# Optimization experiments

Hardware: AMD Instinct MI355X
Metric: run time of the kernel (lower is better)

The kernel has to match this reference:

```python
import jax, jax.numpy as jnp
import numpy as np

N, B, D_IN, HID = 1024, 8, 256, 256
L, SH, LH, GH = 2, 2, 4, 2
H = SH + LH + GH
DH = HID // H
EPS = 1e-5


def _sinusoidal_pe(n, d):
    pos = np.arange(n, dtype=np.float32)[:, None]
    i = np.arange(d, dtype=np.float32)[None, :]
    angle = pos / np.power(10000.0, (2.0 * np.floor(i / 2.0)) / d)
    pe = np.where((np.arange(d) % 2) == 0, np.sin(angle), np.cos(angle))
    return jnp.asarray(pe, jnp.float32)  # (n, d)


def _ln(x, g, b):
    mu = x.mean(-1, keepdims=True)
    var = ((x - mu) ** 2).mean(-1, keepdims=True)
    return (x - mu) * jax.lax.rsqrt(var + EPS) * g + b


def setup_inputs() -> dict:
    key = jax.random.key(0)
    ks = jax.random.split(key, 16)
    s = 0.02
    inp = {
        "nodes": jax.random.normal(ks[0], (N, B, D_IN), jnp.float32),
        "dist": jax.random.randint(ks[1], (B, N, N), 0, 6, jnp.int32),
        "W_in": jax.random.normal(ks[2], (D_IN, HID), jnp.float32) * s,
        "b_in": jnp.zeros((HID,), jnp.float32),
        "ln_in_g": jnp.ones((HID,), jnp.float32),
        "ln_in_b": jnp.zeros((HID,), jnp.float32),
        "Wqkv": jax.random.normal(ks[3], (L, HID, 3 * HID), jnp.float32) * s,
        "bqkv": jnp.zeros((L, 3 * HID), jnp.float32),
        "Wo": jax.random.normal(ks[4], (L, HID, HID), jnp.float32) * s,
        "bo": jnp.zeros((L, HID), jnp.float32),
        "ln1_g": jnp.ones((L, HID), jnp.float32),
        "ln1_b": jnp.zeros((L, HID), jnp.float32),
        "W1": jax.random.normal(ks[5], (L, HID, 2 * HID), jnp.float32) * s,
        "b1": jnp.zeros((L, 2 * HID), jnp.float32),
        "W2": jax.random.normal(ks[6], (L, 2 * HID, HID), jnp.float32) * s,
        "b2": jnp.zeros((L, HID), jnp.float32),
        "ln2_g": jnp.ones((L, HID), jnp.float32),
        "ln2_b": jnp.zeros((L, HID), jnp.float32),
        "bn_g": jnp.ones((HID,), jnp.float32),
        "bn_b": jnp.zeros((HID,), jnp.float32),
    }
    return inp


def reference(nodes, dist, W_in, b_in, ln_in_g, ln_in_b, Wqkv, bqkv, Wo, bo,
              ln1_g, ln1_b, W1, b1, W2, b2, ln2_g, ln2_b, bn_g, bn_b):
    # positional embedding (sinusoidal, added) + dense + LayerNorm; dropout=eval (identity)
    x = nodes + _sinusoidal_pe(N, D_IN)[:, None, :]          # (N,B,D_IN)
    x = _ln(x @ W_in + b_in, ln_in_g, ln_in_b)               # (N,B,HID)

    # dist_to_mask: per-head-group allowed patterns; True in torch mask = disallowed
    short = (dist == 1)[:, None]                             # (B,1,N,N)
    longm = (dist >= 1)[:, None]
    allowed = jnp.concatenate([
        jnp.broadcast_to(short, (B, SH, N, N)),
        jnp.broadcast_to(longm, (B, LH, N, N)),
        jnp.ones((B, GH, N, N), bool),
    ], axis=1)                                               # (B,H,N,N)
    bias = jnp.where(allowed, 0.0, -jnp.inf).astype(x.dtype)

    scale = 1.0 / np.sqrt(DH)
    for l in range(L):
        qkv = x @ Wqkv[l] + bqkv[l]                          # (N,B,3*HID)
        q, k, v = jnp.split(qkv, 3, axis=-1)
        def heads(t):  # (N,B,HID) -> (B,H,N,DH)
            return t.reshape(N, B, H, DH).transpose(1, 2, 0, 3)
        q, k, v = heads(q), heads(k), heads(v)
        s = jnp.einsum('bhnd,bhmd->bhnm', q, k) * scale + bias
        a = jax.nn.softmax(s, axis=-1)
        o = jnp.einsum('bhnm,bhmd->bhnd', a, v)              # (B,H,N,DH)
        o = o.transpose(2, 0, 1, 3).reshape(N, B, HID)
        x = _ln(x + o @ Wo[l] + bo[l], ln1_g[l], ln1_b[l])   # post-norm
        f = jax.nn.relu(x @ W1[l] + b1[l]) @ W2[l] + b2[l]
        x = _ln(x + f, ln2_g[l], ln2_b[l])

    y = x[0]                                                 # (B,HID) first position
    mu = y.mean(0)
    var = ((y - mu) ** 2).mean(0)
    return (y - mu) * jax.lax.rsqrt(var + EPS) * bn_g + bn_b
```

## Files before the change

### kernel.cpp

```cpp
#include <hip/hip_runtime.h>
#include <math.h>

constexpr int Nn = 1024, Bb = 8, HIDc = 256, Hh = 8, DHc = 32;

typedef __bf16 bf16x8 __attribute__((ext_vector_type(8)));
typedef __bf16 bf16x4 __attribute__((ext_vector_type(4)));
typedef float  f32x4  __attribute__((ext_vector_type(4)));

struct WCvtArgs {
    const float* src[9];
    int K[9], M[9], dstOff[9], tiles[9];
};

__global__ __launch_bounds__(256)
void prep_k(WCvtArgs a, __bf16* __restrict__ Wt,
            const int* __restrict__ dist, unsigned char* __restrict__ mp,
            const float* __restrict__ nodes, __bf16* __restrict__ xinb)
{
    __shared__ float ts[32][33];
    const int tid = threadIdx.x;
    if (blockIdx.x < 1088) {
        int bid = blockIdx.x, i = 0;
        while (bid >= a.tiles[i]) { bid -= a.tiles[i]; ++i; }
        const int K = a.K[i], M = a.M[i];
        const int tilesM = M >> 5;
        const int m0 = (bid % tilesM) << 5, k0 = (bid / tilesM) << 5;
        const float* src = a.src[i];
        __bf16* dst = Wt + a.dstOff[i];
        const int tx = tid & 31, ty = tid >> 5;
        #pragma unroll
        for (int j = 0; j < 4; ++j)
            ts[ty + 8 * j][tx] = src[(size_t)(k0 + ty + 8 * j) * M + m0 + tx];
        __syncthreads();
        #pragma unroll
        for (int j = 0; j < 4; ++j)
            dst[(size_t)(m0 + ty + 8 * j) * K + k0 + tx] = (__bf16)ts[tx][ty + 8 * j];
    } else if (blockIdx.x < 3136) {
        const int idx = (blockIdx.x - 1088) * 256 + tid;
        const int quad = idx & 3, c = (idx >> 2) & 15, q = (idx >> 6) & 1023, b = idx >> 16;
        const int* dp = dist + ((((size_t)b << 10) + q) << 10) + c * 64 + quad * 4;
        uchar4 out;
        unsigned char* po = &out.x;
        #pragma unroll
        for (int t = 0; t < 4; ++t) {
            const int4 v = *(const int4*)(dp + t * 16);
            unsigned int code = 0;
            const int dd[4] = {v.x, v.y, v.z, v.w};
            #pragma unroll
            for (int r = 0; r < 4; ++r)
                code |= ((dd[r] == 1 ? 1u : 0u) | (dd[r] >= 1 ? 2u : 0u)) << (2 * r);
            po[t] = (unsigned char)code;
        }
        *(uchar4*)(mp + ((((size_t)b << 10) + q) << 8) + (c << 4) + (quad << 2)) = out;
    } else {
        const int idx = (blockIdx.x - 3136) * 256 + tid;
        const int token = idx >> 7, k2 = (idx & 127) * 2;
        const int b = token >> 10, n = token & 1023;
        const float e = (float)k2 * (1.0f / 256.0f);
        const float freq = exp2f(-13.287712379549449f * e);
        const float ang = (float)n * freq;
        const float2 nd = *(const float2*)(nodes + ((size_t)(n * 8 + b)) * 256 + k2);
        __bf16* p = xinb + (size_t)token * 256 + k2;
        p[0] = (__bf16)(nd.x + sinf(ang));
        p[1] = (__bf16)(nd.y + cosf(ang));
    }
}

template<int NCH>
__device__ __forceinline__ void gemm4(const bf16x8* af, const __bf16* __restrict__ wsrc,
                                      __bf16 (*wlds)[256][72], int mrow, int kcol,
                                      int cq, int col, int quad, f32x4* acc)
{
    constexpr int K = NCH * 64;
    bf16x8 wreg[8];
    #pragma unroll
    for (int i = 0; i < 8; ++i)
        wreg[i] = *(const bf16x8*)(wsrc + (size_t)(i * 32 + mrow) * K + kcol);
    __syncthreads();
    #pragma unroll
    for (int i = 0; i < 8; ++i)
        *(bf16x8*)&wlds[0][i * 32 + mrow][kcol] = wreg[i];
    if (NCH > 1) {
        #pragma unroll
        for (int i = 0; i < 8; ++i)
            wreg[i] = *(const bf16x8*)(wsrc + (size_t)(i * 32 + mrow) * K + 64 + kcol);
    }
    __syncthreads();
    #pragma unroll
    for (int t = 0; t < 4; ++t) acc[t] = (f32x4){0.f, 0.f, 0.f, 0.f};
    for (int ck = 0; ck < NCH; ++ck) {
        #pragma unroll
        for (int t = 0; t < 4; ++t)
            #pragma unroll
            for (int kc = 0; kc < 2; ++kc) {
                const bf16x8 bfr = *(const bf16x8*)(&wlds[ck & 1][cq * 64 + t * 16 + col][kc * 32 + quad * 8]);
                acc[t] = __builtin_amdgcn_mfma_f32_16x16x32_bf16(af[ck * 2 + kc], bfr, acc[t], 0, 0, 0);
            }
        if (ck + 1 < NCH) {
            #pragma unroll
            for (int i = 0; i < 8; ++i)
                *(bf16x8*)&wlds[(ck + 1) & 1][i * 32 + mrow][kcol] = wreg[i];
            if (ck + 2 < NCH) {
                #pragma unroll
                for (int i = 0; i < 8; ++i)
                    wreg[i] = *(const bf16x8*)(wsrc + (size_t)(i * 32 + mrow) * K + (ck + 2) * 64 + kcol);
            }
        }
        __syncthreads();
    }
}

template<bool RESID, bool FFN, bool QKV, bool N0ROWS, bool XGATE, bool BNOUT>
__global__ __launch_bounds__(256)
void layer_k(const __bf16* __restrict__ Ain, const float* __restrict__ xres,
             const __bf16* __restrict__ w0, const float* __restrict__ b0,
             const float* __restrict__ g1, const float* __restrict__ be1,
             const __bf16* __restrict__ w1, const float* __restrict__ b1_,
             const __bf16* __restrict__ w2, const float* __restrict__ b2_,
             const float* __restrict__ g2, const float* __restrict__ be2,
             const __bf16* __restrict__ wq, const float* __restrict__ bq, int qfull,
             const float* __restrict__ bng, const float* __restrict__ bnb,
             float* __restrict__ xout,
             __bf16* __restrict__ qb, __bf16* __restrict__ kb, __bf16* __restrict__ vtb)
{
    __shared__ char smem[73728];
    __bf16 (*wlds)[256][72] = (__bf16 (*)[256][72])smem;
    __bf16 (*trans)[520] = (__bf16 (*)[520])smem;
    __shared__ float red[4][16][2];

    const int tid = threadIdx.x;
    const int lane = tid & 63;
    const int cq = tid >> 6;
    const int col = lane & 15, quad = lane >> 4;
    const int row0 = blockIdx.x * 16;
    const int rowL = col;
    const int mrow = tid >> 3, kcol = (tid & 7) * 8;

    const int rowAg = N0ROWS ? ((col & 7) << 10) : (row0 + col);

    bf16x8 afA[8];
    #pragma unroll
    for (int kc = 0; kc < 8; ++kc)
        afA[kc] = *(const bf16x8*)(Ain + (size_t)rowAg * 256 + kc * 32 + quad * 8);
    f32x4 acc[4];
    gemm4<4>(afA, w0, wlds, mrow, kcol, cq, col, quad, acc);

    float val[4][4];
    {
        float bb[4], gm[4], bt[4];
        #pragma unroll
        for (int t = 0; t < 4; ++t) {
            const int cc = cq * 64 + t * 16 + col;
            bb[t] = b0[cc]; gm[t] = g1[cc]; bt[t] = be1[cc];
        }
        #pragma unroll
        for (int r = 0; r < 4; ++r) {
            const int rl = quad * 4 + r;
            const int rg = N0ROWS ? ((rl & 7) << 10) : (row0 + rl);
            float s1 = 0.f, s2 = 0.f;
            #pragma unroll
            for (int t = 0; t < 4; ++t) {
                float v = acc[t][r] + bb[t];
                if (RESID) v += xres[(size_t)rg * 256 + cq * 64 + t * 16 + col];
                val[r][t] = v; s1 += v; s2 += v * v;
            }
            s1 += __shfl_xor(s1, 1); s1 += __shfl_xor(s1, 2);
            s1 += __shfl_xor(s1, 4); s1 += __shfl_xor(s1, 8);
            s2 += __shfl_xor(s2, 1); s2 += __shfl_xor(s2, 2);
            s2 += __shfl_xor(s2, 4); s2 += __shfl_xor(s2, 8);
            if (col == 0) { red[cq][rl][0] = s1; red[cq][rl][1] = s2; }
        }
        __syncthreads();
        #pragma unroll
        for (int r = 0; r < 4; ++r) {
            const int rl = quad * 4 + r;
            const float s1 = red[0][rl][0] + red[1][rl][0] + red[2][rl][0] + red[3][rl][0];
            const float s2 = red[0][rl][1] + red[1][rl][1] + red[2][rl][1] + red[3][rl][1];
            const float mu = s1 * (1.0f / 256.0f);
            const float rv = rsqrtf(s2 * (1.0f / 256.0f) - mu * mu + 1e-5f);
            #pragma unroll
            for (int t = 0; t < 4; ++t) {
                const float o = (val[r][t] - mu) * rv * gm[t] + bt[t];
                val[r][t] = o;
                trans[rl][cq * 64 + t * 16 + col] = (__bf16)o;
                if (!FFN)
                    xout[(size_t)(row0 + rl) * 256 + cq * 64 + t * 16 + col] = o;
            }
        }
        __syncthreads();
    }

    if (FFN) {
        bf16x8 af1[8];
        #pragma unroll
        for (int kc = 0; kc < 8; ++kc)
            af1[kc] = *(const bf16x8*)(&trans[rowL][kc * 32 + quad * 8]);
        bf16x4 h1p[2][4];
        #pragma unroll
        for (int mh = 0; mh < 2; ++mh) {
            f32x4 accb[4];
            gemm4<4>(af1, w1 + (size_t)mh * 256 * 256, wlds, mrow, kcol, cq, col, quad, accb);
            #pragma unroll
            for (int t = 0; t < 4; ++t) {
                const float bbv = b1_[mh * 256 + cq * 64 + t * 16 + col];
                #pragma unroll
                for (int r = 0; r < 4; ++r)
                    h1p[mh][t][r] = (__bf16)fmaxf(accb[t][r] + bbv, 0.f);
            }
        }
        __syncthreads();
        #pragma unroll
        for (int mh = 0; mh < 2; ++mh)
            #pragma unroll
            for (int t = 0; t < 4; ++t)
                #pragma unroll
                for (int r = 0; r < 4; ++r)
                    trans[quad * 4 + r][mh * 256 + cq * 64 + t * 16 + col] = h1p[mh][t][r];
        __syncthreads();

        bf16x8 af2[16];
        #pragma unroll
        for (int kc = 0; kc < 16; ++kc)
            af2[kc] = *(const bf16x8*)(&trans[rowL][kc * 32 + quad * 8]);
        f32x4 accc[4];
        gemm4<8>(af2, w2, wlds, mrow, kcol, cq, col, quad, accc);

        float bb[4], gm[4], bt[4];
        #pragma unroll
        for (int t = 0; t < 4; ++t) {
            const int cc = cq * 64 + t * 16 + col;
            bb[t] = b2_[cc]; gm[t] = g2[cc]; bt[t] = be2[cc];
        }
        #pragma unroll
        for (int r = 0; r < 4; ++r) {
            const int rl = quad * 4 + r;
            float s1 = 0.f, s2 = 0.f;
            #pragma unroll
            for (int t = 0; t < 4; ++t) {
                const float v = accc[t][r] + bb[t] + val[r][t];
                val[r][t] = v; s1 += v; s2 += v * v;
            }
            s1 += __shfl_xor(s1, 1); s1 += __shfl_xor(s1, 2);
            s1 += __shfl_xor(s1, 4); s1 += __shfl_xor(s1, 8);
            s2 += __shfl_xor(s2, 1); s2 += __shfl_xor(s2, 2);
            s2 += __shfl_xor(s2, 4); s2 += __shfl_xor(s2, 8);
            if (col == 0) { red[cq][rl][0] = s1; red[cq][rl][1] = s2; }
        }
        __syncthreads();
        #pragma unroll
        for (int r = 0; r < 4; ++r) {
            const int rl = quad * 4 + r;
            const float s1 = red[0][rl][0] + red[1][rl][0] + red[2][rl][0] + red[3][rl][0];
            const float s2 = red[0][rl][1] + red[1][rl][1] + red[2][rl][1] + red[3][rl][1];
            const float mu = s1 * (1.0f / 256.0f);
            const float rv = rsqrtf(s2 * (1.0f / 256.0f) - mu * mu + 1e-5f);
            const int rg = N0ROWS ? ((rl & 7) << 10) : (row0 + rl);
            #pragma unroll
            for (int t = 0; t < 4; ++t) {
                const float o = (val[r][t] - mu) * rv * gm[t] + bt[t];
                val[r][t] = o;
                if (QKV) trans[rl][cq * 64 + t * 16 + col] = (__bf16)o;
                if (!BNOUT) {
                    const bool wr = XGATE ? ((rg & 1023) == 0) : true;
                    if (wr) xout[(size_t)rg * 256 + cq * 64 + t * 16 + col] = o;
                }
            }
        }
        if (BNOUT) {
            #pragma unroll
            for (int t = 0; t < 4; ++t) {
                const int cc = cq * 64 + t * 16 + col;
                float s1 = val[0][t] + val[1][t] + val[2][t] + val[3][t];
                float s2 = val[0][t] * val[0][t] + val[1][t] * val[1][t]
                         + val[2][t] * val[2][t] + val[3][t] * val[3][t];
                s1 += __shfl_xor(s1, 16);
                s2 += __shfl_xor(s2, 16);
                const float mu = s1 * 0.125f;
                const float rv = rsqrtf(s2 * 0.125f - mu * mu + 1e-5f);
                const float gg = bng[cc], bb2 = bnb[cc];
                if (quad < 2) {
                    #pragma unroll
                    for (int r = 0; r < 4; ++r)
                        xout[(size_t)(quad * 4 + r) * 256 + cc] = (val[r][t] - mu) * rv * gg + bb2;
                }
            }
        }
        __syncthreads();
    }

    if (QKV) {
        bf16x8 af3[8];
        #pragma unroll
        for (int kc = 0; kc < 8; ++kc)
            af3[kc] = *(const bf16x8*)(&trans[rowL][kc * 32 + quad * 8]);
        const int bq_ = row0 >> 10;
        const int n0q = (row0 & 1023) + quad * 4;
        const bool qneed = qfull || ((row0 & 1023) < 128);
        for (int cg = 0; cg < 3; ++cg) {
            if (cg == 0 && !qneed) continue;
            f32x4 accq[4];
            gemm4<4>(af3, wq + (size_t)cg * 256 * 256, wlds, mrow, kcol, cq, col, quad, accq);
            if (cg == 2) {
                #pragma unroll
                for (int t = 0; t < 4; ++t) {
                    const int cc = cq * 64 + t * 16 + col;
                    const int h = cc >> 5, dh = cc & 31;
                    const float bbv = bq[512 + cc];
                    bf16x4 p;
                    #pragma unroll
                    for (int r = 0; r < 4; ++r) p[r] = (__bf16)(accq[t][r] + bbv);
                    *(bf16x4*)(vtb + ((((size_t)(bq_ * 8 + h)) * 32 + dh) << 10) + n0q) = p;
                }
            } else {
                const float qs = (cg == 0) ? 0.25505402616305625f : 1.0f;
                __bf16* dst = (cg == 0) ? qb : kb;
                #pragma unroll
                for (int t = 0; t < 4; ++t) {
                    const int cc = cq * 64 + t * 16 + col;
                    const int h = cc >> 5, dh = cc & 31;
                    const float bbv = bq[cg * 256 + cc];
                    #pragma unroll
                    for (int r = 0; r < 4; ++r)
                        dst[((((size_t)(bq_ * 8 + h)) << 10) + n0q + r) * 32 + dh] =
                            (__bf16)((accq[t][r] + bbv) * qs);
                }
            }
        }
    }
}

__global__ __launch_bounds__(256)
void attn_mfma(const __bf16* __restrict__ Qb, const __bf16* __restrict__ Kb,
               const __bf16* __restrict__ Vt, const unsigned char* __restrict__ MP,
               __bf16* __restrict__ O)
{
    __shared__ __bf16 pbuf[2][4][2][16][72];
    const int tid = threadIdx.x;
    const int lane = tid & 63;
    const int wv = tid >> 6;
    const int col = lane & 15;
    const int quad = lane >> 4;
    const int xr = blockIdx.x;
    const int bh = ((xr & 7) << 3) | (xr >> 3);
    const int b = bh >> 3, h = bh & 7;
    const int qbase = blockIdx.y * 128 + wv * 32;
    const int hsel = (h < 2) ? 0 : 1;
    const bool masked = (h < 6);

    bf16x8 qf[2];
    #pragma unroll
    for (int j = 0; j < 2; ++j)
        qf[j] = *(const bf16x8*)(Qb + ((size_t)bh * Nn + qbase + j * 16 + col) * DHc + quad * 8);

    bf16x8 onesf;
    {
        const __bf16 one = (__bf16)1.0f, zero = (__bf16)0.0f;
        #pragma unroll
        for (int j = 0; j < 8; ++j) onesf[j] = (col == 0) ? one : zero;
    }

    f32x4 O0[2], O1[2], OL[2];
    #pragma unroll
    for (int j = 0; j < 2; ++j) {
        O0[j] = (f32x4){0.f, 0.f, 0.f, 0.f};
        O1[j] = (f32x4){0.f, 0.f, 0.f, 0.f};
        OL[j] = (f32x4){0.f, 0.f, 0.f, 0.f};
    }
    const f32x4 zf = {0.f, 0.f, 0.f, 0.f};
    const __bf16* kbase = Kb + (size_t)bh * Nn * DHc;

    bf16x8 kf[4];
    #pragma unroll
    for (int t = 0; t < 4; ++t)
        kf[t] = *(const bf16x8*)(kbase + (size_t)(t * 16 + col) * DHc + quad * 8);

    for (int c = 0; c < 16; ++c) {
        bf16x8 kn[4];
        if (c < 15)
            #pragma unroll
            for (int t = 0; t < 4; ++t)
                kn[t] = *(const bf16x8*)(kbase + (size_t)((c + 1) * 64 + t * 16 + col) * DHc + quad * 8);
        uchar4 mk[2];
        if (masked)
            #pragma unroll
            for (int j = 0; j < 2; ++j)
                mk[j] = *(const uchar4*)(MP + ((((size_t)b << 10) + qbase + j * 16 + col) << 8)
                                            + (c << 4) + (quad << 2));
        #pragma unroll
        for (int j = 0; j < 2; ++j) {
            f32x4 S[4];
            #pragma unroll
            for (int t = 0; t < 4; ++t)
                S[t] = __builtin_amdgcn_mfma_f32_16x16x32_bf16(kf[t], qf[j], zf, 0, 0, 0);
            if (masked) {
                const unsigned char mb[4] = {mk[j].x, mk[j].y, mk[j].z, mk[j].w};
                #pragma unroll
                for (int t = 0; t < 4; ++t)
                    #pragma unroll
                    for (int r = 0; r < 4; ++r)
                        if (!((mb[t] >> (2 * r + hsel)) & 1)) S[t][r] = -INFINITY;
            }
            #pragma unroll
            for (int t = 0; t < 4; ++t) {
                bf16x4 p4;
                #pragma unroll
                for (int r = 0; r < 4; ++r)
                    p4[r] = (__bf16)__builtin_amdgcn_exp2f(S[t][r]);
                *(bf16x4*)(&pbuf[c & 1][wv][j][col][t * 16 + quad * 4]) = p4;
            }
        }
        const __bf16* vp = Vt + (size_t)bh * DHc * Nn + c * 64 + quad * 8;
        #pragma unroll
        for (int kh = 0; kh < 2; ++kh) {
            const bf16x8 v0 = *(const bf16x8*)(vp + (size_t)col * Nn + kh * 32);
            const bf16x8 v1 = *(const bf16x8*)(vp + (size_t)(col + 16) * Nn + kh * 32);
            #pragma unroll
            for (int j = 0; j < 2; ++j) {
                const bf16x8 pf = *(const bf16x8*)(&pbuf[c & 1][wv][j][col][kh * 32 + quad * 8]);
                O0[j] = __builtin_amdgcn_mfma_f32_16x16x32_bf16(pf, v0, O0[j], 0, 0, 0);
                O1[j] = __builtin_amdgcn_mfma_f32_16x16x32_bf16(pf, v1, O1[j], 0, 0, 0);
                OL[j] = __builtin_amdgcn_mfma_f32_16x16x32_bf16(pf, onesf, OL[j], 0, 0, 0);
            }
        }
        if (c < 15)
            #pragma unroll
            for (int t = 0; t < 4; ++t) kf[t] = kn[t];
    }
    #pragma unroll
    for (int j = 0; j < 2; ++j)
        #pragma unroll
        for (int r = 0; r < 4; ++r) {
            const float Lr = __shfl(OL[j][r], lane & 48);
            const float inv = 1.0f / Lr;
            const int q = qbase + j * 16 + quad * 4 + r;
            __bf16* op = O + ((size_t)(b * 1024 + q)) * 256 + h * 32 + col;
            op[0]  = (__bf16)(O0[j][r] * inv);
            op[16] = (__bf16)(O1[j][r] * inv);
        }
}

extern "C" void kernel_launch(void* const* d_in, const int* in_sizes, int n_in,
                              void* d_out, int out_size, void* d_ws, size_t ws_size,
                              hipStream_t stream)
{
    const float* nodes   = (const float*)d_in[0];
    const int*   dist    = (const int*)  d_in[1];
    const float* W_in    = (const float*)d_in[2];
    const float* b_in    = (const float*)d_in[3];
    const float* ln_in_g = (const float*)d_in[4];
    const float* ln_in_b = (const float*)d_in[5];
    const float* Wqkv    = (const float*)d_in[6];
    const float* bqkv    = (const float*)d_in[7];
    const float* Wo      = (const float*)d_in[8];
    const float* bo      = (const float*)d_in[9];
    const float* ln1_g   = (const float*)d_in[10];
    const float* ln1_b   = (const float*)d_in[11];
    const float* W1      = (const float*)d_in[12];
    const float* b1      = (const float*)d_in[13];
    const float* W2      = (const float*)d_in[14];
    const float* b2      = (const float*)d_in[15];
    const float* ln2_g   = (const float*)d_in[16];
    const float* ln2_b   = (const float*)d_in[17];
    const float* bn_g    = (const float*)d_in[18];
    const float* bn_b    = (const float*)d_in[19];

    char* ws = (char*)d_ws;
    float*  x   = (float*)(ws);
    unsigned char* mp = (unsigned char*)(ws + 8388608);
    __bf16* wt  = (__bf16*)(ws + 10485760);
    __bf16* qb  = (__bf16*)(ws + 12845056);
    __bf16* kb  = (__bf16*)(ws + 17039360);
    __bf16* vtb = (__bf16*)(ws + 21233664);
    __bf16* ob  = (__bf16*)(ws + 25427968);
    __bf16* xinb = ob;

    WCvtArgs wa;
    wa.src[0] = W_in;           wa.K[0] = 256; wa.M[0] = 256; wa.dstOff[0] = 0;
    wa.src[1] = Wqkv;           wa.K[1] = 256; wa.M[1] = 768; wa.dstOff[1] = 65536;
    wa.src[2] = Wqkv + 196608;  wa.K[2] = 256; wa.M[2] = 768; wa.dstOff[2] = 262144;
    wa.src[3] = Wo;             wa.K[3] = 256; wa.M[3] = 256; wa.dstOff[3] = 458752;
    wa.src[4] = Wo + 65536;     wa.K[4] = 256; wa.M[4] = 256; wa.dstOff[4] = 524288;
    wa.src[5] = W1;             wa.K[5] = 256; wa.M[5] = 512; wa.dstOff[5] = 589824;
    wa.src[6] = W1 + 131072;    wa.K[6] = 256; wa.M[6] = 512; wa.dstOff[6] = 720896;
    wa.src[7] = W2;             wa.K[7] = 512; wa.M[7] = 256; wa.dstOff[7] = 851968;
    wa.src[8] = W2 + 131072;    wa.K[8] = 512; wa.M[8] = 256; wa.dstOff[8] = 983040;
    for (int i = 0; i < 9; ++i) wa.tiles[i] = (wa.K[i] >> 5) * (wa.M[i] >> 5);

    prep_k<<<7232, 256, 0, stream>>>(wa, wt, dist, mp, nodes, xinb);

    layer_k<false, false, true, false, false, false><<<512, 256, 0, stream>>>(
        xinb, nullptr, wt, b_in, ln_in_g, ln_in_b,
        nullptr, nullptr, nullptr, nullptr, nullptr, nullptr,
        wt + 65536, bqkv, 1, nullptr, nullptr, x, qb, kb, vtb);

    attn_mfma<<<dim3(64, 8), 256, 0, stream>>>(qb, kb, vtb, mp, ob);

    layer_k<true, true, true, false, true, false><<<512, 256, 0, stream>>>(
        ob, x, wt + 458752, bo, ln1_g, ln1_b,
        wt + 589824, b1, wt + 851968, b2, ln2_g, ln2_b,
        wt + 262144, bqkv + 768, 0, nullptr, nullptr, x, qb, kb, vtb);

    attn_mfma<<<dim3(64, 1), 256, 0, stream>>>(qb, kb, vtb, mp, ob);

    layer_k<true, true, false, true, true, true><<<1, 256, 0, stream>>>(
        ob, x, wt + 524288, bo + 256, ln1_g + 256, ln1_b + 256,
        wt + 720896, b1 + 512, wt + 983040, b2 + 256, ln2_g + 256, ln2_b + 256,
        nullptr, nullptr, 0, bn_g, bn_b, (float*)d_out, nullptr, nullptr, nullptr);
}
```

Baseline: 254.2 us.

## Stream weights directly into MFMA A-operands and process 32 tokens per block

The fused layer kernel no longer stages weight tiles through double-buffered LDS with barriers. Each wave now loads its weight rows straight from global memory into registers as the MFMA A operand, and reads activations from a small LDS token buffer as the B operand. Each block handles 32 tokens instead of 16, so every weight fragment is reused twice and the grid halves. Epilogues use vectorized float4 loads and stores for bias, LayerNorm and outputs. The aim is to cut LDS traffic and syncs, at the cost of higher register pressure, fewer blocks, and more global weight reads per block (served from cache).

After: 267.3 us. 1.05x slower.

```diff
diff --git a/kernel.cpp b/kernel.cpp
--- a/kernel.cpp
+++ b/kernel.cpp
@@ -2,6 +2,7 @@
 #include <math.h>
 
 constexpr int Nn = 1024, Bb = 8, HIDc = 256, Hh = 8, DHc = 32;
+constexpr int TSTR = 520;
 
 typedef __bf16 bf16x8 __attribute__((ext_vector_type(8)));
 typedef __bf16 bf16x4 __attribute__((ext_vector_type(4)));
@@ -66,51 +67,44 @@
     }
 }
 
-template<int NCH>
-__device__ __forceinline__ void gemm4(const bf16x8* af, const __bf16* __restrict__ wsrc,
-                                      __bf16 (*wlds)[256][72], int mrow, int kcol,
-                                      int cq, int col, int quad, f32x4* acc)
+template<int KK, int NJ>
+__device__ __forceinline__ void gemmT(const __bf16* __restrict__ wrow,
+                                      const __bf16* __restrict__ x0,
+                                      const __bf16* __restrict__ x1,
+                                      f32x4 acc[4][2])
 {
-    constexpr int K = NCH * 64;
-    bf16x8 wreg[8];
-    #pragma unroll
-    for (int i = 0; i < 8; ++i)
-        wreg[i] = *(const bf16x8*)(wsrc + (size_t)(i * 32 + mrow) * K + kcol);
-    __syncthreads();
-    #pragma unroll
-    for (int i = 0; i < 8; ++i)
-        *(bf16x8*)&wlds[0][i * 32 + mrow][kcol] = wreg[i];
-    if (NCH > 1) {
-        #pragma unroll
-        for (int i = 0; i < 8; ++i)
-            wreg[i] = *(const bf16x8*)(wsrc + (size_t)(i * 32 + mrow) * K + 64 + kcol);
-    }
-    __syncthreads();
-    #pragma unroll
-    for (int t = 0; t < 4; ++t) acc[t] = (f32x4){0.f, 0.f, 0.f, 0.f};
-    for (int ck = 0; ck < NCH; ++ck) {
+    constexpr int NKC = KK / 32;
+    bf16x8 wA[4][4];
+    #pragma unroll
+    for (int p = 0; p < 4; ++p)
         #pragma unroll
         for (int t = 0; t < 4; ++t)
-            #pragma unroll
-            for (int kc = 0; kc < 2; ++kc) {
-                const bf16x8 bfr = *(const bf16x8*)(&wlds[ck & 1][cq * 64 + t * 16 + col][kc * 32 + quad * 8]);
-                acc[t] = __builtin_amdgcn_mfma_f32_16x16x32_bf16(af[ck * 2 + kc], bfr, acc[t], 0, 0, 0);
-            }
-        if (ck + 1 < NCH) {
-            #pragma unroll
-            for (int i = 0; i < 8; ++i)
-                *(bf16x8*)&wlds[(ck + 1) & 1][i * 32 + mrow][kcol] = wreg[i];
-            if (ck + 2 < NCH) {
-                #pragma unroll
-                for (int i = 0; i < 8; ++i)
-                    wreg[i] = *(const bf16x8*)(wsrc + (size_t)(i * 32 + mrow) * K + (ck + 2) * 64 + kcol);
-            }
-        }
-        __syncthreads();
+            wA[p][t] = *(const bf16x8*)(wrow + (size_t)(t * 16) * KK + p * 32);
+    #pragma unroll
+    for (int t = 0; t < 4; ++t) {
+        acc[t][0] = (f32x4){0.f, 0.f, 0.f, 0.f};
+        if (NJ == 2) acc[t][1] = (f32x4){0.f, 0.f, 0.f, 0.f};
+    }
+    #pragma unroll
+    for (int kc = 0; kc < NKC; ++kc) {
+        const bf16x8 b0 = *(const bf16x8*)(x0 + kc * 32);
+        bf16x8 b1;
+        if (NJ == 2) b1 = *(const bf16x8*)(x1 + kc * 32);
+        const int cur = kc & 3;
+        #pragma unroll
+        for (int t = 0; t < 4; ++t) {
+            acc[t][0] = __builtin_amdgcn_mfma_f32_16x16x32_bf16(wA[cur][t], b0, acc[t][0], 0, 0, 0);
+            if (NJ == 2)
+                acc[t][1] = __builtin_amdgcn_mfma_f32_16x16x32_bf16(wA[cur][t], b1, acc[t][1], 0, 0, 0);
+        }
+        if (kc + 4 < NKC)
+            #pragma unroll
+            for (int t = 0; t < 4; ++t)
+                wA[cur][t] = *(const bf16x8*)(wrow + (size_t)(t * 16) * KK + (kc + 4) * 32);
     }
 }
 
-template<bool RESID, bool FFN, bool QKV, bool N0ROWS, bool XGATE, bool BNOUT>
+template<bool RESID, bool FFN, bool QKV, bool N0ROWS, bool XGATE, bool BNOUT, int NJ>
 __global__ __launch_bounds__(256)
 void layer_k(const __bf16* __restrict__ Ain, const float* __restrict__ xres,
              const __bf16* __restrict__ w0, const float* __restrict__ b0,
@@ -123,206 +117,231 @@
              float* __restrict__ xout,
              __bf16* __restrict__ qb, __bf16* __restrict__ kb, __bf16* __restrict__ vtb)
 {
-    __shared__ char smem[73728];
-    __bf16 (*wlds)[256][72] = (__bf16 (*)[256][72])smem;
-    __bf16 (*trans)[520] = (__bf16 (*)[520])smem;
-    __shared__ float red[4][16][2];
+    __shared__ __bf16 trans[32][TSTR];
+    __shared__ float red[4][32][2];
 
     const int tid = threadIdx.x;
     const int lane = tid & 63;
     const int cq = tid >> 6;
     const int col = lane & 15, quad = lane >> 4;
-    const int row0 = blockIdx.x * 16;
-    const int rowL = col;
-    const int mrow = tid >> 3, kcol = (tid & 7) * 8;
-
-    const int rowAg = N0ROWS ? ((col & 7) << 10) : (row0 + col);
-
-    bf16x8 afA[8];
-    #pragma unroll
-    for (int kc = 0; kc < 8; ++kc)
-        afA[kc] = *(const bf16x8*)(Ain + (size_t)rowAg * 256 + kc * 32 + quad * 8);
-    f32x4 acc[4];
-    gemm4<4>(afA, w0, wlds, mrow, kcol, cq, col, quad, acc);
-
-    float val[4][4];
+    const int row0 = blockIdx.x * (NJ * 16);
+    const int mb = cq * 64;
+
+    #pragma unroll
+    for (int i = 0; i < 2; ++i) {
+        const int v = i * 256 + tid;
+        const int rw = v >> 4, cc = (v & 15) * 16;
+        const int rg = N0ROWS ? ((rw & 7) << 10) : (row0 + rw);
+        *(bf16x8*)&trans[rw][cc]     = *(const bf16x8*)(Ain + (size_t)rg * 256 + cc);
+        *(bf16x8*)&trans[rw][cc + 8] = *(const bf16x8*)(Ain + (size_t)rg * 256 + cc + 8);
+    }
+    __syncthreads();
+
+    const __bf16* x0 = &trans[col][quad * 8];
+    const __bf16* x1 = &trans[16 + col][quad * 8];
+    int tg[2];
+    #pragma unroll
+    for (int j = 0; j < NJ; ++j)
+        tg[j] = N0ROWS ? ((j * 16 + col) & 7) << 10 : (row0 + j * 16 + col);
+
+    f32x4 acc[4][2];
+    gemmT<256, NJ>(w0 + (size_t)(mb + col) * 256 + quad * 8, x0, x1, acc);
+
+    float val[2][4][4];
     {
-        float bb[4], gm[4], bt[4];
+        float4 bb4[4], gm4[4], bt4[4];
         #pragma unroll
         for (int t = 0; t < 4; ++t) {
-            const int cc = cq * 64 + t * 16 + col;
-            bb[t] = b0[cc]; gm[t] = g1[cc]; bt[t] = be1[cc];
-        }
-        #pragma unroll
-        for (int r = 0; r < 4; ++r) {
-            const int rl = quad * 4 + r;
-            const int rg = N0ROWS ? ((rl & 7) << 10) : (row0 + rl);
+            const int cb = mb + t * 16 + quad * 4;
+            bb4[t] = *(const float4*)&b0[cb];
+            gm4[t] = *(const float4*)&g1[cb];
+            bt4[t] = *(const float4*)&be1[cb];
+        }
+        #pragma unroll
+        for (int j = 0; j < NJ; ++j) {
             float s1 = 0.f, s2 = 0.f;
             #pragma unroll
             for (int t = 0; t < 4; ++t) {
-                float v = acc[t][r] + bb[t];
-                if (RESID) v += xres[(size_t)rg * 256 + cq * 64 + t * 16 + col];
-                val[r][t] = v; s1 += v; s2 += v * v;
-            }
-            s1 += __shfl_xor(s1, 1); s1 += __shfl_xor(s1, 2);
-            s1 += __shfl_xor(s1, 4); s1 += __shfl_xor(s1, 8);
-            s2 += __shfl_xor(s2, 1); s2 += __shfl_xor(s2, 2);
-            s2 += __shfl_xor(s2, 4); s2 += __shfl_xor(s2, 8);
-            if (col == 0) { red[cq][rl][0] = s1; red[cq][rl][1] = s2; }
-        }
-        __syncthreads();
-        #pragma unroll
-        for (int r = 0; r < 4; ++r) {
-            const int rl = quad * 4 + r;
-            const float s1 = red[0][rl][0] + red[1][rl][0] + red[2][rl][0] + red[3][rl][0];
-            const float s2 = red[0][rl][1] + red[1][rl][1] + red[2][rl][1] + red[3][rl][1];
+                float4 xr4 = {0.f, 0.f, 0.f, 0.f};
+                if (RESID) xr4 = *(const float4*)&xres[(size_t)tg[j] * 256 + mb + t * 16 + quad * 4];
+                const float* bbp = (const float*)&bb4[t];
+                const float* xrp = (const float*)&xr4;
+                #pragma unroll
+                for (int r = 0; r < 4; ++r) {
+                    float v = acc[t][j][r] + bbp[r] + xrp[r];
+                    val[j][t][r] = v; s1 += v; s2 += v * v;
+                }
+            }
+            s1 += __shfl_xor(s1, 16); s1 += __shfl_xor(s1, 32);
+            s2 += __shfl_xor(s2, 16); s2 += __shfl_xor(s2, 32);
+            if (quad == 0) { red[cq][j * 16 + col][0] = s1; red[cq][j * 16 + col][1] = s2; }
+        }
+        __syncthreads();
+        #pragma unroll
+        for (int j = 0; j < NJ; ++j) {
+            const int tk = j * 16 + col;
+            const float s1 = red[0][tk][0] + red[1][tk][0] + red[2][tk][0] + red[3][tk][0];
+            const float s2 = red[0][tk][1] + red[1][tk][1] + red[2][tk][1] + red[3][tk][1];
             const float mu = s1 * (1.0f / 256.0f);
             const float rv = rsqrtf(s2 * (1.0f / 256.0f) - mu * mu + 1e-5f);
             #pragma unroll
             for (int t = 0; t < 4; ++t) {
-                const float o = (val[r][t] - mu) * rv * gm[t] + bt[t];
-                val[r][t] = o;
-                trans[rl][cq * 64 + t * 16 + col] = (__bf16)o;
+                const float* gmp = (const float*)&gm4[t];
+                const float* btp = (const float*)&bt4[t];
+                bf16x4 o4; float4 of;
+                #pragma unroll
+                for (int r = 0; r < 4; ++r) {
+                    const float o = (val[j][t][r] - mu) * rv * gmp[r] + btp[r];
+                    val[j][t][r] = o;
+                    o4[r] = (__bf16)o;
+                    ((float*)&of)[r] = o;
+                }
+                *(bf16x4*)&trans[tk][mb + t * 16 + quad * 4] = o4;
                 if (!FFN)
-                    xout[(size_t)(row0 + rl) * 256 + cq * 64 + t * 16 + col] = o;
+                    *(float4*)&xout[(size_t)tg[j] * 256 + mb + t * 16 + quad * 4] = of;
             }
         }
         __syncthreads();
     }
 
     if (FFN) {
-        bf16x8 af1[8];
-        #pragma unroll
-        for (int kc = 0; kc < 8; ++kc)
-            af1[kc] = *(const bf16x8*)(&trans[rowL][kc * 32 + quad * 8]);
-        bf16x4 h1p[2][4];
+        bf16x4 h1p[2][2][4];
         #pragma unroll
         for (int mh = 0; mh < 2; ++mh) {
-            f32x4 accb[4];
-            gemm4<4>(af1, w1 + (size_t)mh * 256 * 256, wlds, mrow, kcol, cq, col, quad, accb);
-            #pragma unroll
-            for (int t = 0; t < 4; ++t) {
-                const float bbv = b1_[mh * 256 + cq * 64 + t * 16 + col];
-                #pragma unroll
-                for (int r = 0; r < 4; ++r)
-                    h1p[mh][t][r] = (__bf16)fmaxf(accb[t][r] + bbv, 0.f);
+            f32x4 a1[4][2];
+            gemmT<256, NJ>(w1 + (size_t)(mh * 256 + mb + col) * 256 + quad * 8, x0, x1, a1);
+            #pragma unroll
+            for (int t = 0; t < 4; ++t) {
+                const float4 bh4 = *(const float4*)&b1_[mh * 256 + mb + t * 16 + quad * 4];
+                const float* bhp = (const float*)&bh4;
+                #pragma unroll
+                for (int j = 0; j < NJ; ++j)
+                    #pragma unroll
+                    for (int r = 0; r < 4; ++r)
+                        h1p[mh][j][t][r] = (__bf16)fmaxf(a1[t][j][r] + bhp[r], 0.f);
             }
         }
         __syncthreads();
         #pragma unroll
         for (int mh = 0; mh < 2; ++mh)
             #pragma unroll
-            for (int t = 0; t < 4; ++t)
-                #pragma unroll
-                for (int r = 0; r < 4; ++r)
-                    trans[quad * 4 + r][mh * 256 + cq * 64 + t * 16 + col] = h1p[mh][t][r];
-        __syncthreads();
-
-        bf16x8 af2[16];
-        #pragma unroll
-        for (int kc = 0; kc < 16; ++kc)
-            af2[kc] = *(const bf16x8*)(&trans[rowL][kc * 32 + quad * 8]);
-        f32x4 accc[4];
-        gemm4<8>(af2, w2, wlds, mrow, kcol, cq, col, quad, accc);
-
-        float bb[4], gm[4], bt[4];
+            for (int j = 0; j < NJ; ++j)
+                #pragma unroll
+                for (int t = 0; t < 4; ++t)
+                    *(bf16x4*)&trans[j * 16 + col][mh * 256 + mb + t * 16 + quad * 4] = h1p[mh][j][t];
+        __syncthreads();
+
+        f32x4 a2[4][2];
+        gemmT<512, NJ>(w2 + (size_t)(mb + col) * 512 + quad * 8, x0, x1, a2);
+
+        float4 bb4[4], gm4[4], bt4[4];
         #pragma unroll
         for (int t = 0; t < 4; ++t) {
-            const int cc = cq * 64 + t * 16 + col;
-            bb[t] = b2_[cc]; gm[t] = g2[cc]; bt[t] = be2[cc];
-        }
-        #pragma unroll
-        for (int r = 0; r < 4; ++r) {
-            const int rl = quad * 4 + r;
+            const int cb = mb + t * 16 + quad * 4;
+            bb4[t] = *(const float4*)&b2_[cb];
+            gm4[t] = *(const float4*)&g2[cb];
+            bt4[t] = *(const float4*)&be2[cb];
+        }
+        #pragma unroll
+        for (int j = 0; j < NJ; ++j) {
             float s1 = 0.f, s2 = 0.f;
             #pragma unroll
             for (int t = 0; t < 4; ++t) {
-                const float v = accc[t][r] + bb[t] + val[r][t];
-                val[r][t] = v; s1 += v; s2 += v * v;
-            }
-            s1 += __shfl_xor(s1, 1); s1 += __shfl_xor(s1, 2);
-            s1 += __shfl_xor(s1, 4); s1 += __shfl_xor(s1, 8);
-            s2 += __shfl_xor(s2, 1); s2 += __shfl_xor(s2, 2);
-            s2 += __shfl_xor(s2, 4); s2 += __shfl_xor(s2, 8);
-            if (col == 0) { red[cq][rl][0] = s1; red[cq][rl][1] = s2; }
-        }
-        __syncthreads();
-        #pragma unroll
-        for (int r = 0; r < 4; ++r) {
-            const int rl = quad * 4 + r;
-            const float s1 = red[0][rl][0] + red[1][rl][0] + red[2][rl][0] + red[3][rl][0];
-            const float s2 = red[0][rl][1] + red[1][rl][1] + red[2][rl][1] + red[3][rl][1];
+                const float* bbp = (const float*)&bb4[t];
+                #pragma unroll
+                for (int r = 0; r < 4; ++r) {
+                    const float v = a2[t][j][r] + bbp[r] + val[j][t][r];
+                    val[j][t][r] = v; s1 += v; s2 += v * v;
+                }
+            }
+            s1 += __shfl_xor(s1, 16); s1 += __shfl_xor(s1, 32);
+            s2 += __shfl_xor(s2, 16); s2 += __shfl_xor(s2, 32);
+            if (quad == 0) { red[cq][j * 16 + col][0] = s1; red[cq][j * 16 + col][1] = s2; }
+        }
+        __syncthreads();
+        #pragma unroll
+        for (int j = 0; j < NJ; ++j) {
+            const int tk = j * 16 + col;
+            const float s1 = red[0][tk][0] + red[1][tk][0] + red[2][tk][0] + red[3][tk][0];
+            const float s2 = red[0][tk][1] + red[1][tk][1] + red[2][tk][1] + red[3][tk][1];
             const float mu = s1 * (1.0f / 256.0f);
             const float rv = rsqrtf(s2 * (1.0f / 256.0f) - mu * mu + 1e-5f);
-            const int rg = N0ROWS ? ((rl & 7) << 10) : (row0 + rl);
-            #pragma unroll
-            for (int t = 0; t < 4; ++t) {
-                const float o = (val[r][t] - mu) * rv * gm[t] + bt[t];
-                val[r][t] = o;
-                if (QKV) trans[rl][cq * 64 + t * 16 + col] = (__bf16)o;
+            #pragma unroll
+            for (int t = 0; t < 4; ++t) {
+                const float* gmp = (const float*)&gm4[t];
+                const float* btp = (const float*)&bt4[t];
+                bf16x4 o4; float4 of;
+                #pragma unroll
+                for (int r = 0; r < 4; ++r) {
+                    const float o = (val[j][t][r] - mu) * rv * gmp[r] + btp[r];
+                    val[j][t][r] = o;
+                    o4[r] = (__bf16)o;
+                    ((float*)&of)[r] = o;
+                }
+                if (QKV) *(bf16x4*)&trans[tk][mb + t * 16 + quad * 4] = o4;
                 if (!BNOUT) {
-                    const bool wr = XGATE ? ((rg & 1023) == 0) : true;
-                    if (wr) xout[(size_t)rg * 256 + cq * 64 + t * 16 + col] = o;
+                    const bool wr = XGATE ? ((tg[j] & 1023) == 0) : true;
+                    if (wr) *(float4*)&xout[(size_t)tg[j] * 256 + mb + t * 16 + quad * 4] = of;
                 }
             }
         }
         if (BNOUT) {
             #pragma unroll
             for (int t = 0; t < 4; ++t) {
-                const int cc = cq * 64 + t * 16 + col;
-                float s1 = val[0][t] + val[1][t] + val[2][t] + val[3][t];
-                float s2 = val[0][t] * val[0][t] + val[1][t] * val[1][t]
-                         + val[2][t] * val[2][t] + val[3][t] * val[3][t];
-                s1 += __shfl_xor(s1, 16);
-                s2 += __shfl_xor(s2, 16);
-                const float mu = s1 * 0.125f;
-                const float rv = rsqrtf(s2 * 0.125f - mu * mu + 1e-5f);
-                const float gg = bng[cc], bb2 = bnb[cc];
-                if (quad < 2) {
-                    #pragma unroll
-                    for (int r = 0; r < 4; ++r)
-                        xout[(size_t)(quad * 4 + r) * 256 + cc] = (val[r][t] - mu) * rv * gg + bb2;
-                }
+                const int cb = mb + t * 16 + quad * 4;
+                const float4 g4 = *(const float4*)&bng[cb];
+                const float4 bB = *(const float4*)&bnb[cb];
+                float4 of;
+                #pragma unroll
+                for (int r = 0; r < 4; ++r) {
+                    float s1 = val[0][t][r], s2 = val[0][t][r] * val[0][t][r];
+                    s1 += __shfl_xor(s1, 1); s2 += __shfl_xor(s2, 1);
+                    s1 += __shfl_xor(s1, 2); s2 += __shfl_xor(s2, 2);
+                    s1 += __shfl_xor(s1, 4); s2 += __shfl_xor(s2, 4);
+                    s1 += __shfl_xor(s1, 8); s2 += __shfl_xor(s2, 8);
+                    const float mu = s1 * (1.0f / 16.0f);
+                    const float rv = rsqrtf(s2 * (1.0f / 16.0f) - mu * mu + 1e-5f);
+                    ((float*)&of)[r] = (val[0][t][r] - mu) * rv * ((const float*)&g4)[r]
+                                       + ((const float*)&bB)[r];
+                }
+                if (col < 8)
+                    *(float4*)&xout[(size_t)col * 256 + cb] = of;
             }
         }
         __syncthreads();
     }
 
     if (QKV) {
-        bf16x8 af3[8];
-        #pragma unroll
-        for (int kc = 0; kc < 8; ++kc)
-            af3[kc] = *(const bf16x8*)(&trans[rowL][kc * 32 + quad * 8]);
-        const int bq_ = row0 >> 10;
-        const int n0q = (row0 & 1023) + quad * 4;
+        const int b_ = N0ROWS ? 0 : (row0 >> 10);
         const bool qneed = qfull || ((row0 & 1023) < 128);
         for (int cg = 0; cg < 3; ++cg) {
             if (cg == 0 && !qneed) continue;
-            f32x4 accq[4];
-            gemm4<4>(af3, wq + (size_t)cg * 256 * 256, wlds, mrow, kcol, cq, col, quad, accq);
-            if (cg == 2) {
-                #pragma unroll
-                for (int t = 0; t < 4; ++t) {
-                    const int cc = cq * 64 + t * 16 + col;
-                    const int h = cc >> 5, dh = cc & 31;
-                    const float bbv = bq[512 + cc];
-                    bf16x4 p;
-                    #pragma unroll
-                    for (int r = 0; r < 4; ++r) p[r] = (__bf16)(accq[t][r] + bbv);
-                    *(bf16x4*)(vtb + ((((size_t)(bq_ * 8 + h)) * 32 + dh) << 10) + n0q) = p;
-                }
-            } else {
-                const float qs = (cg == 0) ? 0.25505402616305625f : 1.0f;
-                __bf16* dst = (cg == 0) ? qb : kb;
-                #pragma unroll
-                for (int t = 0; t < 4; ++t) {
-                    const int cc = cq * 64 + t * 16 + col;
-                    const int h = cc >> 5, dh = cc & 31;
-                    const float bbv = bq[cg * 256 + cc];
-                    #pragma unroll
-                    for (int r = 0; r < 4; ++r)
-                        dst[((((size_t)(bq_ * 8 + h)) << 10) + n0q + r) * 32 + dh] =
-                            (__bf16)((accq[t][r] + bbv) * qs);
+            f32x4 aq[4][2];
+            gemmT<256, NJ>(wq + (size_t)(cg * 256 + mb + col) * 256 + quad * 8, x0, x1, aq);
+            const float qs = (cg == 0) ? 0.25505402616305625f : 1.0f;
+            #pragma unroll
+            for (int t = 0; t < 4; ++t) {
+                const int cc = mb + t * 16;
+                const int h = cc >> 5;
+                const int dhb = (cc & 31) + quad * 4;
+                const float4 bq4 = *(const float4*)&bq[cg * 256 + cc + quad * 4];
+                const float* bqp = (const float*)&bq4;
+                #pragma unroll
+                for (int j = 0; j < NJ; ++j) {
+                    const int n = tg[j] & 1023;
+                    if (cg == 2) {
+                        #pragma unroll
+                        for (int r = 0; r < 4; ++r)
+                            vtb[((size_t)(b_ * 8 + h) * 32 + dhb + r) * 1024 + n] =
+                                (__bf16)(aq[t][j][r] + bqp[r]);
+                    } else {
+                        bf16x4 p;
+                        #pragma unroll
+                        for (int r = 0; r < 4; ++r)
+                            p[r] = (__bf16)((aq[t][j][r] + bqp[r]) * qs);
+                        __bf16* dst = (cg == 0) ? qb : kb;
+                        *(bf16x4*)&dst[((size_t)(b_ * 8 + h) * 1024 + n) * 32 + dhb] = p;
+                    }
                 }
             }
         }
@@ -393,12 +412,12 @@
             for (int t = 0; t < 4; ++t)
                 S[t] = __builtin_amdgcn_mfma_f32_16x16x32_bf16(kf[t], qf[j], zf, 0, 0, 0);
             if (masked) {
-                const unsigned char mb[4] = {mk[j].x, mk[j].y, mk[j].z, mk[j].w};
+                const unsigned char mb2[4] = {mk[j].x, mk[j].y, mk[j].z, mk[j].w};
                 #pragma unroll
                 for (int t = 0; t < 4; ++t)
                     #pragma unroll
                     for (int r = 0; r < 4; ++r)
-                        if (!((mb[t] >> (2 * r + hsel)) & 1)) S[t][r] = -INFINITY;
+                        if (!((mb2[t] >> (2 * r + hsel)) & 1)) S[t][r] = -INFINITY;
             }
             #pragma unroll
             for (int t = 0; t < 4; ++t) {
@@ -488,21 +507,21 @@
 
     prep_k<<<7232, 256, 0, stream>>>(wa, wt, dist, mp, nodes, xinb);
 
-    layer_k<false, false, true, false, false, false><<<512, 256, 0, stream>>>(
+    layer_k<false, false, true, false, false, false, 2><<<256, 256, 0, stream>>>(
         xinb, nullptr, wt, b_in, ln_in_g, ln_in_b,
         nullptr, nullptr, nullptr, nullptr, nullptr, nullptr,
         wt + 65536, bqkv, 1, nullptr, nullptr, x, qb, kb, vtb);
 
     attn_mfma<<<dim3(64, 8), 256, 0, stream>>>(qb, kb, vtb, mp, ob);
 
-    layer_k<true, true, true, false, true, false><<<512, 256, 0, stream>>>(
+    layer_k<true, true, true, false, true, false, 2><<<256, 256, 0, stream>>>(
         ob, x, wt + 458752, bo, ln1_g, ln1_b,
         wt + 589824, b1, wt + 851968, b2, ln2_g, ln2_b,
         wt + 262144, bqkv + 768, 0, nullptr, nullptr, x, qb, kb, vtb);
 
     attn_mfma<<<dim3(64, 1), 256, 0, stream>>>(qb, kb, vtb, mp, ob);
 
-    layer_k<true, true, false, true, true, true><<<1, 256, 0, stream>>>(
+    layer_k<true, true, false, true, true, true, 1><<<1, 256, 0, stream>>>(
         ob, x, wt + 524288, bo + 256, ln1_g + 256, ln1_b + 256,
         wt + 720896, b1 + 512, wt + 983040, b2 + 256, ln2_g + 256, ln2_b + 256,
         nullptr, nullptr, 0, bn_g, bn_b, (float*)d_out, nullptr, nullptr, nullptr);
```
